# Performance work log

Measured on AMD Instinct MI355X. Metric: run time of the kernel, lower is better.

The kernel has to match this reference:

```python
import jax, jax.numpy as jnp
import numpy as np

N = 100000
E = 1000000
F_IN = 128
HID = 64
HEADS = 4
NC = 4


def setup_inputs() -> dict:
    key = jax.random.key(0)
    ks = jax.random.split(key, 24)
    s = 0.05
    inp = {
        "x": jax.random.normal(ks[0], (N, F_IN), jnp.float32),
        "edge_index": jax.random.randint(ks[1], (2, E), 0, N, jnp.int64 if jax.config.jax_enable_x64 else jnp.int32),
        "edge_weight": jax.random.uniform(ks[2], (E,), jnp.float32),
        "node_mask": jnp.ones((N,), jnp.bool_),
        # GCNConv: lin (no bias applied pre-propagate in math below; bias added after)
        "gcn_W": s * jax.random.normal(ks[3], (F_IN, HID), jnp.float32),
        "gcn_b": jnp.zeros((HID,), jnp.float32),
        "proj_W": s * jax.random.normal(ks[4], (F_IN, HID), jnp.float32),
        "proj_b": jnp.zeros((HID,), jnp.float32),
        "ln1_g": jnp.ones((HID,), jnp.float32), "ln1_b": jnp.zeros((HID,), jnp.float32),
        # GATv2Conv heads=4, concat=False: lin_l, lin_r -> [F, H*C], att [H, C], bias [C]
        "gat_Wl": s * jax.random.normal(ks[5], (HID, HEADS * HID), jnp.float32),
        "gat_Wr": s * jax.random.normal(ks[6], (HID, HEADS * HID), jnp.float32),
        "gat_att": s * jax.random.normal(ks[7], (HEADS, HID), jnp.float32),
        "gat_b": jnp.zeros((HID,), jnp.float32),
        "ln2_g": jnp.ones((HID,), jnp.float32), "ln2_b": jnp.zeros((HID,), jnp.float32),
        # SAGEConv: lin_l (neighbors, with bias), lin_r (root, no bias)
        "sage_Wl": s * jax.random.normal(ks[8], (HID, HID), jnp.float32),
        "sage_bl": jnp.zeros((HID,), jnp.float32),
        "sage_Wr": s * jax.random.normal(ks[9], (HID, HID), jnp.float32),
        "ln3_g": jnp.ones((HID,), jnp.float32), "ln3_b": jnp.zeros((HID,), jnp.float32),
        # edge MLP: Linear(2*HID+1, 32) -> ReLU -> Linear(32, 1)
        "emlp_W1": s * jax.random.normal(ks[10], (2 * HID + 1, 32), jnp.float32),
        "emlp_b1": jnp.zeros((32,), jnp.float32),
        "emlp_W2": s * jax.random.normal(ks[11], (32, 1), jnp.float32),
        "emlp_b2": jnp.zeros((1,), jnp.float32),
        # heads on JK-cat dim 3*HID
        "mort_W": s * jax.random.normal(ks[12], (3 * HID, 1), jnp.float32),
        "mort_b": jnp.zeros((1,), jnp.float32),
        "hours_W": s * jax.random.normal(ks[13], (3 * HID, 1), jnp.float32),
        "hours_b": jnp.zeros((1,), jnp.float32),
        "disc_W": s * jax.random.normal(ks[14], (3 * HID, NC), jnp.float32),
        "disc_b": jnp.zeros((NC,), jnp.float32),
    }
    return inp


def _ln(h, g, b, eps=1e-5):
    mu = jnp.mean(h, axis=-1, keepdims=True)
    var = jnp.mean(jnp.square(h - mu), axis=-1, keepdims=True)
    return (h - mu) * jax.lax.rsqrt(var + eps) * g + b


def reference(x, edge_index, edge_weight, node_mask,
              gcn_W, gcn_b, proj_W, proj_b, ln1_g, ln1_b,
              gat_Wl, gat_Wr, gat_att, gat_b, ln2_g, ln2_b,
              sage_Wl, sage_bl, sage_Wr, ln3_g, ln3_b,
              emlp_W1, emlp_b1, emlp_W2, emlp_b2,
              mort_W, mort_b, hours_W, hours_b, disc_W, disc_b):
    n = x.shape[0]
    src, dst = edge_index[0], edge_index[1]
    loop = jnp.arange(n, dtype=src.dtype)
    s2 = jnp.concatenate([src, loop])  # edges + self loops (GCN, GATv2)
    d2 = jnp.concatenate([dst, loop])

    # ---- GCNConv (normalized, self loops with weight 1) ----
    w2 = jnp.concatenate([edge_weight, jnp.ones((n,), x.dtype)])
    deg = jax.ops.segment_sum(w2, d2, num_segments=n)
    dinv = jnp.where(deg > 0, jax.lax.rsqrt(deg), 0.0)
    norm = dinv[s2] * w2 * dinv[d2]
    xw = x @ gcn_W  # [N, HID]
    gcn_out = jax.ops.segment_sum(norm[:, None] * xw[s2], d2, num_segments=n) + gcn_b
    h1 = jax.nn.relu(_ln(gcn_out, ln1_g, ln1_b))
    h_init = h1 + (x @ proj_W + proj_b)

    # ---- edge-gated edge MLP (recomputed weights; unused by later convs, kept for fidelity) ----
    feat = jnp.concatenate([h_init[src], h_init[dst], edge_weight[:, None]], axis=1)
    _new_ew = jax.nn.sigmoid((jax.nn.relu(feat @ emlp_W1 + emlp_b1) @ emlp_W2 + emlp_b2)[:, 0])

    # ---- GATv2Conv (heads=4, concat=False -> mean over heads, self loops) ----
    H, C = gat_att.shape
    xl = (h_init @ gat_Wl).reshape(n, H, C)
    xr = (h_init @ gat_Wr).reshape(n, H, C)
    e = jax.nn.leaky_relu(xl[s2] + xr[d2], 0.2)        # [E+N, H, C]
    score = jnp.einsum('ehc,hc->eh', e, gat_att)        # [E+N, H]
    smax = jax.ops.segment_max(score, d2, num_segments=n)
    ex = jnp.exp(score - smax[d2])
    den = jax.ops.segment_sum(ex, d2, num_segments=n)
    alpha = ex / den[d2]
    gat_out = jax.ops.segment_sum(alpha[:, :, None] * xl[s2], d2, num_segments=n)
    gat_out = jnp.mean(gat_out, axis=1) + gat_b
    h2 = jax.nn.relu(_ln(gat_out, ln2_g, ln2_b)) + h_init

    # ---- SAGEConv (mean aggregation, root weight, no self loops) ----
    nsum = jax.ops.segment_sum(h2[src], dst, num_segments=n)
    cnt = jax.ops.segment_sum(jnp.ones(src.shape, h2.dtype), dst, num_segments=n)
    nmean = nsum / jnp.maximum(cnt, 1.0)[:, None]
    sage_out = nmean @ sage_Wl + sage_bl + h2 @ sage_Wr
    h3 = jax.nn.relu(_ln(sage_out, ln3_g, ln3_b)) + h2

    # ---- JumpingKnowledge cat + masked readout + heads ----
    x_jk = jnp.concatenate([h_init, h2, h3], axis=1)  # [N, 3*HID]
    readout = jnp.where(node_mask[:, None], x_jk, 0.0)
    mort = (readout @ mort_W + mort_b)[:, 0]
    hours = (readout @ hours_W + hours_b)[:, 0]
    disc = readout @ disc_W + disc_b
    return mort, hours, disc
```

## Files before the change

### kernel.cpp

```cpp
#include <hip/hip_runtime.h>
#include <hip/hip_fp16.h>
#include <math.h>

#define N_NODES 100000
#define N_EDGES 1000000
#define F_IN    128
#define HID     64
#define HEADS   4
#define NCLS    4
#define SCAN_BLK 98
#define GEMM_NT 5

typedef _Float16 half8 __attribute__((ext_vector_type(8)));
typedef _Float16 fp16x2 __attribute__((ext_vector_type(2)));
typedef float f32x4 __attribute__((ext_vector_type(4)));

__device__ __forceinline__ float wsum(float v) {
#pragma unroll
  for (int o = 32; o > 0; o >>= 1) v += __shfl_xor(v, o, 64);
  return v;
}
struct Half4 { __half2 a, b; };
__device__ __forceinline__ __half2 absh2(__half2 v) {
  unsigned u; __builtin_memcpy(&u, &v, 4);
  u &= 0x7FFF7FFFu;
  __half2 r; __builtin_memcpy(&r, &u, 4);
  return r;
}
__device__ __forceinline__ float fdot2f(__half2 a, __half2 b, float c) {
#if defined(__has_builtin) && __has_builtin(__builtin_amdgcn_fdot2)
  fp16x2 av, bv;
  __builtin_memcpy(&av, &a, 4); __builtin_memcpy(&bv, &b, 4);
  return __builtin_amdgcn_fdot2(av, bv, c, false);
#else
  float2 af = __half22float2(a), bf = __half22float2(b);
  return c + af.x * bf.x + af.y * bf.y;
#endif
}
__device__ __forceinline__ float edge_score(Half4 A, __half2 Ra, __half2 Rb,
                                            __half2 at0, __half2 at1,
                                            __half2 c06, __half2 c04) {
  __half2 t0 = __hadd2(A.a, Ra), t1 = __hadd2(A.b, Rb);
  __half2 l0 = __hfma2(t0, c06, __hmul2(absh2(t0), c04));
  __half2 l1 = __hfma2(t1, c06, __hmul2(absh2(t1), c04));
  return fdot2f(l1, at1, fdot2f(l0, at0, 0.f));
}
__device__ __forceinline__ float reduce16(float q) {
  q += __shfl_xor(q, 1); q += __shfl_xor(q, 2);
  q += __shfl_xor(q, 4); q += __shfl_xor(q, 8);
  return q;
}
__device__ __forceinline__ int wave_node() {
  return __builtin_amdgcn_readfirstlane(blockIdx.x * 4 + (threadIdx.x >> 6));
}

__global__ void k_hist(const int* __restrict__ dst, int* __restrict__ cnt) {
  int e = blockIdx.x * 256 + threadIdx.x;
  if (e < N_EDGES) atomicAdd(&cnt[dst[e]], 1);
}
__global__ __launch_bounds__(256) void k_scan1(const int* __restrict__ cnt,
                                               int* __restrict__ partial,
                                               int* __restrict__ bsum) {
  __shared__ int lds[256];
  int t = threadIdx.x;
  int base = blockIdx.x * 1024 + t * 4;
  int v0 = (base + 0 < N_NODES) ? cnt[base + 0] : 0;
  int v1 = (base + 1 < N_NODES) ? cnt[base + 1] : 0;
  int v2 = (base + 2 < N_NODES) ? cnt[base + 2] : 0;
  int v3 = (base + 3 < N_NODES) ? cnt[base + 3] : 0;
  int s = v0 + v1 + v2 + v3;
  lds[t] = s;
  __syncthreads();
  for (int o = 1; o < 256; o <<= 1) {
    int x = (t >= o) ? lds[t - o] : 0;
    __syncthreads();
    lds[t] += x;
    __syncthreads();
  }
  int excl = lds[t] - s;
  if (base + 0 < N_NODES) partial[base + 0] = excl;
  if (base + 1 < N_NODES) partial[base + 1] = excl + v0;
  if (base + 2 < N_NODES) partial[base + 2] = excl + v0 + v1;
  if (base + 3 < N_NODES) partial[base + 3] = excl + v0 + v1 + v2;
  if (t == 255) bsum[blockIdx.x] = lds[255];
}
__global__ void k_scan2(int* __restrict__ bsum) {
  __shared__ int lds[128];
  int t = threadIdx.x;
  int v = (t < SCAN_BLK) ? bsum[t] : 0;
  lds[t] = v;
  __syncthreads();
  for (int o = 1; o < 128; o <<= 1) {
    int x = (t >= o) ? lds[t - o] : 0;
    __syncthreads();
    lds[t] += x;
    __syncthreads();
  }
  if (t < SCAN_BLK) bsum[t] = lds[t] - v;
}
__global__ void k_scan3(const int* __restrict__ partial, const int* __restrict__ bsum,
                        int* __restrict__ row_ptr, int* __restrict__ cursor) {
  int i = blockIdx.x * 256 + threadIdx.x;
  if (i < N_NODES) {
    int v = partial[i] + bsum[i >> 10];
    row_ptr[i] = v;
    cursor[i] = v;
  }
  if (i == 0) row_ptr[N_NODES] = N_EDGES;
}
__global__ void k_fill(const int* __restrict__ src, const int* __restrict__ dst,
                       const float* __restrict__ ew, int* __restrict__ cursor,
                       int* __restrict__ csr_src, float* __restrict__ csr_w) {
  int e = blockIdx.x * 256 + threadIdx.x;
  if (e >= N_EDGES) return;
  int d = dst[e];
  int p = atomicAdd(&cursor[d], 1);
  csr_src[p] = src[e];
  csr_w[p] = ew[e];
}

__global__ __launch_bounds__(512) void k_in_gemm_mfma(
    const float* __restrict__ x, const float* __restrict__ gcn_W,
    const float* __restrict__ proj_W, const float* __restrict__ proj_b,
    __half* __restrict__ xw16, float* __restrict__ xp) {
  __shared__ __half at[16 * 136];
  int t = threadIdx.x;
  int w = t >> 6, lane = t & 63;
  int m = lane & 15, q = lane >> 4;
  int ncol = w * 16 + m;
  const float* W = (ncol < 64) ? gcn_W : proj_W;
  int nc = (ncol < 64) ? ncol : ncol - 64;
  half8 bf[4];
#pragma unroll
  for (int ch = 0; ch < 4; ++ch) {
    int kb = ch * 32 + q * 8;
#pragma unroll
    for (int j = 0; j < 8; ++j)
      bf[ch][j] = (_Float16)W[(kb + j) * 64 + nc];
  }
  float pb = (ncol >= 64) ? proj_b[nc] : 0.f;
  int nb0 = blockIdx.x * (16 * GEMM_NT);
  for (int nt = 0; nt < GEMM_NT; ++nt) {
    int nb = nb0 + nt * 16;
    {
      int row = t >> 5, col = (t & 31) * 4;
      float4 v = *reinterpret_cast<const float4*>(x + (size_t)(nb + row) * F_IN + col);
      __half2* d = reinterpret_cast<__half2*>(&at[row * 136 + col]);
      d[0] = __floats2half2_rn(v.x, v.y);
      d[1] = __floats2half2_rn(v.z, v.w);
    }
    __syncthreads();
    f32x4 acc = {0.f, 0.f, 0.f, 0.f};
#pragma unroll
    for (int ch = 0; ch < 4; ++ch) {
      half8 af = *reinterpret_cast<const half8*>(&at[m * 136 + ch * 32 + q * 8]);
      acc = __builtin_amdgcn_mfma_f32_16x16x32_f16(af, bf[ch], acc, 0, 0, 0);
    }
    if (ncol < 64) {
#pragma unroll
      for (int r = 0; r < 4; ++r)
        xw16[(size_t)(nb + q * 4 + r) * HID + nc] = __float2half(acc[r]);
    } else {
#pragma unroll
      for (int r = 0; r < 4; ++r)
        xp[(size_t)(nb + q * 4 + r) * HID + nc] = acc[r] + pb;
    }
    __syncthreads();
  }
}

__global__ void k_deg(const int* __restrict__ row_ptr, const float* __restrict__ csr_w,
                      float* __restrict__ dinv) {
  int n = blockIdx.x * 256 + threadIdx.x;
  if (n >= N_NODES) return;
  float deg = 1.0f;
  int end = row_ptr[n + 1];
  for (int i = row_ptr[n]; i < end; ++i) deg += csr_w[i];
  dinv[n] = rsqrtf(deg);
}

__global__ __launch_bounds__(256) void k_gcn_fused(
    const int* __restrict__ row_ptr, const int* __restrict__ csr_src,
    const float* __restrict__ csr_w, const float* __restrict__ dinv,
    const __half* __restrict__ xw16, const float* __restrict__ xp,
    const float* __restrict__ gcn_b, const float* __restrict__ g,
    const float* __restrict__ bb, __half* __restrict__ h_init16) {
  int n = wave_node();
  int lane = threadIdx.x & 63;
  float di = dinv[n];
  float acc = di * di * __half2float(xw16[(size_t)n * HID + lane]);
  int beg = row_ptr[n], end = row_ptr[n + 1];
  int i = beg;
  for (; i + 4 <= end; i += 4) {
    int s0 = __builtin_amdgcn_readfirstlane(csr_src[i]);
    int s1 = __builtin_amdgcn_readfirstlane(csr_src[i + 1]);
    int s2 = __builtin_amdgcn_readfirstlane(csr_src[i + 2]);
    int s3 = __builtin_amdgcn_readfirstlane(csr_src[i + 3]);
    float nrm0 = dinv[s0] * csr_w[i] * di;
    float nrm1 = dinv[s1] * csr_w[i + 1] * di;
    float nrm2 = dinv[s2] * csr_w[i + 2] * di;
    float nrm3 = dinv[s3] * csr_w[i + 3] * di;
    float v0 = __half2float(xw16[(size_t)s0 * HID + lane]);
    float v1 = __half2float(xw16[(size_t)s1 * HID + lane]);
    float v2 = __half2float(xw16[(size_t)s2 * HID + lane]);
    float v3 = __half2float(xw16[(size_t)s3 * HID + lane]);
    acc += nrm0 * v0 + nrm1 * v1 + nrm2 * v2 + nrm3 * v3;
  }
  for (; i < end; ++i) {
    int s = __builtin_amdgcn_readfirstlane(csr_src[i]);
    float nrm = dinv[s] * csr_w[i] * di;
    acc += nrm * __half2float(xw16[(size_t)s * HID + lane]);
  }
  float v = acc + gcn_b[lane];
  float mu = wsum(v) * (1.f / HID);
  float dv = v - mu;
  float var = wsum(dv * dv) * (1.f / HID);
  float h = dv * rsqrtf(var + 1e-5f) * g[lane] + bb[lane];
  h = h > 0.f ? h : 0.f;
  h_init16[(size_t)n * HID + lane] = __float2half(h + xp[(size_t)n * HID + lane]);
}

__global__ __launch_bounds__(512) void k_gat_gemm_mfma(
    const __half* __restrict__ h16, const float* __restrict__ Wl,
    const float* __restrict__ Wr, __half* __restrict__ xl, __half* __restrict__ xr) {
  __shared__ __half at[16 * 72];
  int t = threadIdx.x;
  int w = t >> 6, lane = t & 63;
  int m = lane & 15, q = lane >> 4;
  half8 bf[4][2];
#pragma unroll
  for (int tt = 0; tt < 4; ++tt) {
    int c = w * 16 + tt * 128 + m;
    const float* W = (c < 256) ? Wl : Wr;
    int nc = (c < 256) ? c : c - 256;
#pragma unroll
    for (int ch = 0; ch < 2; ++ch) {
      int kb = ch * 32 + q * 8;
#pragma unroll
      for (int j = 0; j < 8; ++j)
        bf[tt][ch][j] = (_Float16)W[(kb + j) * 256 + nc];
    }
  }
  int nb0 = blockIdx.x * (16 * GEMM_NT);
  for (int nt = 0; nt < GEMM_NT; ++nt) {
    int nb = nb0 + nt * 16;
    {
      int row = t >> 5, col = (t & 31) * 2;
      *reinterpret_cast<__half2*>(&at[row * 72 + col]) =
          *reinterpret_cast<const __half2*>(h16 + (size_t)(nb + row) * HID + col);
    }
    __syncthreads();
    half8 a0 = *reinterpret_cast<const half8*>(&at[m * 72 + q * 8]);
    half8 a1 = *reinterpret_cast<const half8*>(&at[m * 72 + 32 + q * 8]);
#pragma unroll
    for (int tt = 0; tt < 4; ++tt) {
      f32x4 acc = {0.f, 0.f, 0.f, 0.f};
      acc = __builtin_amdgcn_mfma_f32_16x16x32_f16(a0, bf[tt][0], acc, 0, 0, 0);
      acc = __builtin_amdgcn_mfma_f32_16x16x32_f16(a1, bf[tt][1], acc, 0, 0, 0);
      int c = w * 16 + tt * 128 + m;
      __half* out = (c < 256) ? (xl + c) : (xr + (c - 256));
#pragma unroll
      for (int r = 0; r < 4; ++r)
        out[(size_t)(nb + q * 4 + r) * 256] = __float2half(acc[r]);
    }
    __syncthreads();
  }
}

__global__ __launch_bounds__(256) void k_gat_fused(
    const int* __restrict__ row_ptr, const int* __restrict__ csr_src,
    const __half* __restrict__ xl, const __half* __restrict__ xr,
    const float* __restrict__ att, const float* __restrict__ gat_b,
    const float* __restrict__ g, const float* __restrict__ bb,
    const __half* __restrict__ h_init16, __half* __restrict__ h2_16) {
  int n = wave_node();
  int lane = threadIdx.x & 63;
  const __half2 c06 = __float2half2_rn(0.6f);
  const __half2 c04 = __float2half2_rn(0.4f);
  float4 atv = *reinterpret_cast<const float4*>(att + lane * 4);
  __half2 at0 = __floats2half2_rn(atv.x, atv.y);
  __half2 at1 = __floats2half2_rn(atv.z, atv.w);
  Half4 R = *reinterpret_cast<const Half4*>(xr + (size_t)n * 256 + lane * 4);
  Half4 S = *reinterpret_cast<const Half4*>(xl + (size_t)n * 256 + lane * 4);

  float q = reduce16(edge_score(S, R.a, R.b, at0, at1, c06, c04));
  float w = __expf(q);
  float den = w;
  float2 f0 = __half22float2(S.a), f1 = __half22float2(S.b);
  float4 acc = make_float4(w * f0.x, w * f0.y, w * f1.x, w * f1.y);

  int beg = row_ptr[n], end = row_ptr[n + 1];
  int i = beg;
  for (; i + 4 <= end; i += 4) {
    int s0 = __builtin_amdgcn_readfirstlane(csr_src[i]);
    int s1 = __builtin_amdgcn_readfirstlane(csr_src[i + 1]);
    int s2 = __builtin_amdgcn_readfirstlane(csr_src[i + 2]);
    int s3 = __builtin_amdgcn_readfirstlane(csr_src[i + 3]);
    Half4 A0 = *reinterpret_cast<const Half4*>(xl + (size_t)s0 * 256 + lane * 4);
    Half4 A1 = *reinterpret_cast<const Half4*>(xl + (size_t)s1 * 256 + lane * 4);
    Half4 A2 = *reinterpret_cast<const Half4*>(xl + (size_t)s2 * 256 + lane * 4);
    Half4 A3 = *reinterpret_cast<const Half4*>(xl + (size_t)s3 * 256 + lane * 4);
    float q0 = edge_score(A0, R.a, R.b, at0, at1, c06, c04);
    float q1 = edge_score(A1, R.a, R.b, at0, at1, c06, c04);
    float q2 = edge_score(A2, R.a, R.b, at0, at1, c06, c04);
    float q3 = edge_score(A3, R.a, R.b, at0, at1, c06, c04);
    q0 += __shfl_xor(q0, 1); q1 += __shfl_xor(q1, 1);
    q2 += __shfl_xor(q2, 1); q3 += __shfl_xor(q3, 1);
    q0 += __shfl_xor(q0, 2); q1 += __shfl_xor(q1, 2);
    q2 += __shfl_xor(q2, 2); q3 += __shfl_xor(q3, 2);
    q0 += __shfl_xor(q0, 4); q1 += __shfl_xor(q1, 4);
    q2 += __shfl_xor(q2, 4); q3 += __shfl_xor(q3, 4);
    q0 += __shfl_xor(q0, 8); q1 += __shfl_xor(q1, 8);
    q2 += __shfl_xor(q2, 8); q3 += __shfl_xor(q3, 8);
    float w0 = __expf(q0), w1 = __expf(q1);
    float w2 = __expf(q2), w3 = __expf(q3);
    den += (w0 + w1) + (w2 + w3);
    float2 a00 = __half22float2(A0.a), a01 = __half22float2(A0.b);
    float2 a10 = __half22float2(A1.a), a11 = __half22float2(A1.b);
    float2 a20 = __half22float2(A2.a), a21 = __half22float2(A2.b);
    float2 a30 = __half22float2(A3.a), a31 = __half22float2(A3.b);
    acc.x += (w0 * a00.x + w1 * a10.x) + (w2 * a20.x + w3 * a30.x);
    acc.y += (w0 * a00.y + w1 * a10.y) + (w2 * a20.y + w3 * a30.y);
    acc.z += (w0 * a01.x + w1 * a11.x) + (w2 * a21.x + w3 * a31.x);
    acc.w += (w0 * a01.y + w1 * a11.y) + (w2 * a21.y + w3 * a31.y);
  }
  for (; i < end; ++i) {
    int s0 = __builtin_amdgcn_readfirstlane(csr_src[i]);
    Half4 A0 = *reinterpret_cast<const Half4*>(xl + (size_t)s0 * 256 + lane * 4);
    q = reduce16(edge_score(A0, R.a, R.b, at0, at1, c06, c04));
    w = __expf(q);
    den += w;
    float2 a00 = __half22float2(A0.a), a01 = __half22float2(A0.b);
    acc.x += w * a00.x; acc.y += w * a00.y;
    acc.z += w * a01.x; acc.w += w * a01.y;
  }
  float inv = 1.f / den;
  acc.x *= inv; acc.y *= inv; acc.z *= inv; acc.w *= inv;
  acc.x += __shfl_xor(acc.x, 16); acc.y += __shfl_xor(acc.y, 16);
  acc.z += __shfl_xor(acc.z, 16); acc.w += __shfl_xor(acc.w, 16);
  acc.x += __shfl_xor(acc.x, 32); acc.y += __shfl_xor(acc.y, 32);
  acc.z += __shfl_xor(acc.z, 32); acc.w += __shfl_xor(acc.w, 32);
  int srcl = lane >> 2;
  float t0 = __shfl(acc.x, srcl), t1 = __shfl(acc.y, srcl);
  float t2 = __shfl(acc.z, srcl), t3 = __shfl(acc.w, srcl);
  int r = lane & 3;
  float mean = (r == 0) ? t0 : (r == 1) ? t1 : (r == 2) ? t2 : t3;
  float val = mean * 0.25f + gat_b[lane];
  float mu = wsum(val) * (1.f / HID);
  float dv = val - mu;
  float var = wsum(dv * dv) * (1.f / HID);
  float h = dv * rsqrtf(var + 1e-5f) * g[lane] + bb[lane];
  h = h > 0.f ? h : 0.f;
  float outv = h + __half2float(h_init16[(size_t)n * HID + lane]);
  h2_16[(size_t)n * HID + lane] = __float2half(outv);
}

__global__ __launch_bounds__(256) void k_sage_gather(
    const int* __restrict__ row_ptr, const int* __restrict__ csr_src,
    const __half* __restrict__ h2_16, float* __restrict__ nmean) {
  int n = wave_node();
  int lane = threadIdx.x & 63;
  int beg = row_ptr[n], end = row_ptr[n + 1];
  float sum = 0.f;
  int i = beg;
  for (; i + 4 <= end; i += 4) {
    int s0 = __builtin_amdgcn_readfirstlane(csr_src[i]);
    int s1 = __builtin_amdgcn_readfirstlane(csr_src[i + 1]);
    int s2 = __builtin_amdgcn_readfirstlane(csr_src[i + 2]);
    int s3 = __builtin_amdgcn_readfirstlane(csr_src[i + 3]);
    float v0 = __half2float(h2_16[(size_t)s0 * HID + lane]);
    float v1 = __half2float(h2_16[(size_t)s1 * HID + lane]);
    float v2 = __half2float(h2_16[(size_t)s2 * HID + lane]);
    float v3 = __half2float(h2_16[(size_t)s3 * HID + lane]);
    sum += v0 + v1 + v2 + v3;
  }
  for (; i < end; ++i) {
    int s = __builtin_amdgcn_readfirstlane(csr_src[i]);
    sum += __half2float(h2_16[(size_t)s * HID + lane]);
  }
  nmean[(size_t)n * HID + lane] = sum / fmaxf((float)(end - beg), 1.f);
}

__global__ __launch_bounds__(64) void k_sage_gemm_ln(
    const float* __restrict__ nmean, const __half* __restrict__ h2_16,
    const float* __restrict__ Wl, const float* __restrict__ Wr,
    const float* __restrict__ sage_bl, const float* __restrict__ g,
    const float* __restrict__ bb, float* __restrict__ h3) {
  __shared__ float nt[8][HID];
  __shared__ float ht[8][HID];
  int t = threadIdx.x;
  int n0 = blockIdx.x * 8;
  {
    const float4* ng = reinterpret_cast<const float4*>(nmean + (size_t)n0 * HID);
    float4* ns = reinterpret_cast<float4*>(&nt[0][0]);
    ns[t] = ng[t];
    ns[t + 64] = ng[t + 64];
    const __half* hp = h2_16 + (size_t)n0 * HID + t * 8;
    Half4 p0 = *reinterpret_cast<const Half4*>(hp);
    Half4 p1 = *reinterpret_cast<const Half4*>(hp + 4);
    float* dsth = &ht[0][0] + t * 8;
    float2 f;
    f = __half22float2(p0.a); dsth[0] = f.x; dsth[1] = f.y;
    f = __half22float2(p0.b); dsth[2] = f.x; dsth[3] = f.y;
    f = __half22float2(p1.a); dsth[4] = f.x; dsth[5] = f.y;
    f = __half22float2(p1.b); dsth[6] = f.x; dsth[7] = f.y;
  }
  __syncthreads();
  int f = t;
  float acc[8] = {0.f,0.f,0.f,0.f,0.f,0.f,0.f,0.f};
  for (int k = 0; k < HID; k += 4) {
    float wl0 = Wl[(k + 0) * HID + f], wr0 = Wr[(k + 0) * HID + f];
    float wl1 = Wl[(k + 1) * HID + f], wr1 = Wr[(k + 1) * HID + f];
    float wl2 = Wl[(k + 2) * HID + f], wr2 = Wr[(k + 2) * HID + f];
    float wl3 = Wl[(k + 3) * HID + f], wr3 = Wr[(k + 3) * HID + f];
#pragma unroll
    for (int j = 0; j < 8; ++j) {
      float4 nv = *reinterpret_cast<const float4*>(&nt[j][k]);
      float4 hv = *reinterpret_cast<const float4*>(&ht[j][k]);
      acc[j] += nv.x * wl0 + nv.y * wl1 + nv.z * wl2 + nv.w * wl3
              + hv.x * wr0 + hv.y * wr1 + hv.z * wr2 + hv.w * wr3;
    }
  }
  float blv = sage_bl[f], gv = g[f], bbv = bb[f];
#pragma unroll
  for (int j = 0; j < 8; ++j) {
    float v = acc[j] + blv;
    float mu = wsum(v) * (1.f / HID);
    float dv = v - mu;
    float var = wsum(dv * dv) * (1.f / HID);
    float h = dv * rsqrtf(var + 1e-5f) * gv + bbv;
    h = h > 0.f ? h : 0.f;
    h3[(size_t)(n0 + j) * HID + f] = h + ht[j][f];
  }
}

__global__ __launch_bounds__(256) void k_heads(
    const __half* __restrict__ h_init16, const __half* __restrict__ h2_16,
    const float* __restrict__ h3, const int* __restrict__ mask,
    const float* __restrict__ mort_W, const float* __restrict__ mort_b,
    const float* __restrict__ hours_W, const float* __restrict__ hours_b,
    const float* __restrict__ disc_W, const float* __restrict__ disc_b,
    float* __restrict__ out) {
  int n = wave_node();
  int lane = threadIdx.x & 63;
  float m = (mask[n] != 0) ? 1.f : 0.f;
  size_t base = (size_t)n * HID;
  float v0 = __half2float(h_init16[base + lane]) * m;
  float v1 = __half2float(h2_16[base + lane]) * m;
  float v2 = h3[base + lane] * m;
  float pm = v0 * mort_W[lane] + v1 * mort_W[64 + lane] + v2 * mort_W[128 + lane];
  float ph = v0 * hours_W[lane] + v1 * hours_W[64 + lane] + v2 * hours_W[128 + lane];
  float d0 = v0 * disc_W[lane * 4 + 0] + v1 * disc_W[(64 + lane) * 4 + 0] + v2 * disc_W[(128 + lane) * 4 + 0];
  float d1 = v0 * disc_W[lane * 4 + 1] + v1 * disc_W[(64 + lane) * 4 + 1] + v2 * disc_W[(128 + lane) * 4 + 1];
  float d2 = v0 * disc_W[lane * 4 + 2] + v1 * disc_W[(64 + lane) * 4 + 2] + v2 * disc_W[(128 + lane) * 4 + 2];
  float d3 = v0 * disc_W[lane * 4 + 3] + v1 * disc_W[(64 + lane) * 4 + 3] + v2 * disc_W[(128 + lane) * 4 + 3];
  pm = wsum(pm); ph = wsum(ph);
  d0 = wsum(d0); d1 = wsum(d1); d2 = wsum(d2); d3 = wsum(d3);
  if (lane == 0) {
    out[n] = pm + mort_b[0];
    out[N_NODES + n] = ph + hours_b[0];
    float* dd = out + 2 * N_NODES + (size_t)n * 4;
    dd[0] = d0 + disc_b[0];
    dd[1] = d1 + disc_b[1];
    dd[2] = d2 + disc_b[2];
    dd[3] = d3 + disc_b[3];
  }
}

extern "C" void kernel_launch(void* const* d_in, const int* in_sizes, int n_in,
                              void* d_out, int out_size, void* d_ws, size_t ws_size,
                              hipStream_t stream) {
  const float* x       = (const float*)d_in[0];
  const int*   ei      = (const int*)d_in[1];
  const float* ew      = (const float*)d_in[2];
  const int*   mask    = (const int*)d_in[3];
  const float* gcn_W   = (const float*)d_in[4];
  const float* gcn_b   = (const float*)d_in[5];
  const float* proj_W  = (const float*)d_in[6];
  const float* proj_b  = (const float*)d_in[7];
  const float* ln1_g   = (const float*)d_in[8];
  const float* ln1_b   = (const float*)d_in[9];
  const float* gat_Wl  = (const float*)d_in[10];
  const float* gat_Wr  = (const float*)d_in[11];
  const float* gat_att = (const float*)d_in[12];
  const float* gat_b   = (const float*)d_in[13];
  const float* ln2_g   = (const float*)d_in[14];
  const float* ln2_b   = (const float*)d_in[15];
  const float* sage_Wl = (const float*)d_in[16];
  const float* sage_bl = (const float*)d_in[17];
  const float* sage_Wr = (const float*)d_in[18];
  const float* ln3_g   = (const float*)d_in[19];
  const float* ln3_b   = (const float*)d_in[20];
  const float* mort_W  = (const float*)d_in[25];
  const float* mort_b  = (const float*)d_in[26];
  const float* hours_W = (const float*)d_in[27];
  const float* hours_b = (const float*)d_in[28];
  const float* disc_W  = (const float*)d_in[29];
  const float* disc_b  = (const float*)d_in[30];

  const int* src = ei;
  const int* dst = ei + N_EDGES;
  float* out = (float*)d_out;

  float* ws = (float*)d_ws;
  const size_t F = (size_t)N_NODES * HID;
  float* h3     = ws + 2 * F;
  float* xp     = h3;
  __half* xl    = (__half*)(ws + 3 * F);
  __half* xw16  = xl;
  float* nmean  = ws + 3 * F;
  __half* xr    = (__half*)(ws + 3 * F + (size_t)N_NODES * 128);
  __half* h2_16 = (__half*)(ws + 3 * F + (size_t)N_NODES * 256);
  __half* h_init16 = (__half*)(ws + 3 * F + (size_t)N_NODES * 288);
  float* tail   = ws + 3 * F + (size_t)N_NODES * 320;
  int*   csr_src = (int*)tail;           tail += N_EDGES;
  float* csr_w   = tail;                 tail += N_EDGES;
  int*   row_ptr = (int*)tail;           tail += N_NODES + 64;
  int*   cursor  = (int*)tail;           tail += N_NODES;
  int*   cnt     = (int*)tail;           tail += N_NODES;
  int*   partial = (int*)tail;           tail += N_NODES;
  int*   bsum    = (int*)tail;           tail += 128;
  float* dinv    = tail;

  const int GE = (N_EDGES + 255) / 256;
  const int GN = (N_NODES + 255) / 256;
  const int GB = N_NODES / (16 * GEMM_NT);

  hipMemsetAsync(cnt, 0, N_NODES * sizeof(int), stream);
  k_hist<<<GE, 256, 0, stream>>>(dst, cnt);
  k_scan1<<<SCAN_BLK, 256, 0, stream>>>(cnt, partial, bsum);
  k_scan2<<<1, 128, 0, stream>>>(bsum);
  k_scan3<<<GN, 256, 0, stream>>>(partial, bsum, row_ptr, cursor);
  k_fill<<<GE, 256, 0, stream>>>(src, dst, ew, cursor, csr_src, csr_w);

  k_in_gemm_mfma<<<GB, 512, 0, stream>>>(x, gcn_W, proj_W, proj_b, xw16, xp);
  k_deg<<<GN, 256, 0, stream>>>(row_ptr, csr_w, dinv);
  k_gcn_fused<<<N_NODES / 4, 256, 0, stream>>>(row_ptr, csr_src, csr_w, dinv, xw16,
                                               xp, gcn_b, ln1_g, ln1_b, h_init16);

  k_gat_gemm_mfma<<<GB, 512, 0, stream>>>(h_init16, gat_Wl, gat_Wr, xl, xr);
  k_gat_fused<<<N_NODES / 4, 256, 0, stream>>>(row_ptr, csr_src, xl, xr, gat_att,
                                               gat_b, ln2_g, ln2_b, h_init16, h2_16);

  k_sage_gather<<<N_NODES / 4, 256, 0, stream>>>(row_ptr, csr_src, h2_16, nmean);
  k_sage_gemm_ln<<<N_NODES / 8, 64, 0, stream>>>(nmean, h2_16, sage_Wl, sage_Wr,
                                                 sage_bl, ln3_g, ln3_b, h3);

  k_heads<<<N_NODES / 4, 256, 0, stream>>>(h_init16, h2_16, h3, mask, mort_W, mort_b,
                                           hours_W, hours_b, disc_W, disc_b, out);
}
```

Baseline: 571.7 us.

## Fuse readout heads into SAGE GEMM, fold scan2 into scan3, store fp16 intermediates

Merges the block-sum scan into the final scan kernel, so each block rescans the 98 block sums in LDS and one launch is dropped. The projection output and the SAGE neighbour mean are now stored as fp16 instead of fp32, which halves their memory traffic. The heads kernel is fused into the SAGE GEMM+LayerNorm kernel, so h3 is never written to or read back from global memory. The cost is lower precision on two intermediates and redundant scan work in every scan3 block.

Measured after the change: 566.4 us. No clear change (-0.9%).

```diff
diff --git a/kernel.cpp b/kernel.cpp
--- a/kernel.cpp
+++ b/kernel.cpp
@@ -84,25 +84,29 @@
   if (base + 3 < N_NODES) partial[base + 3] = excl + v0 + v1 + v2;
   if (t == 255) bsum[blockIdx.x] = lds[255];
 }
-__global__ void k_scan2(int* __restrict__ bsum) {
-  __shared__ int lds[128];
+__global__ __launch_bounds__(256) void k_scan3(const int* __restrict__ partial,
+                                               const int* __restrict__ bsum,
+                                               int* __restrict__ row_ptr,
+                                               int* __restrict__ cursor) {
+  __shared__ int ex[128];
   int t = threadIdx.x;
-  int v = (t < SCAN_BLK) ? bsum[t] : 0;
-  lds[t] = v;
+  int orig = 0;
+  if (t < 128) {
+    orig = (t < SCAN_BLK) ? bsum[t] : 0;
+    ex[t] = orig;
+  }
   __syncthreads();
   for (int o = 1; o < 128; o <<= 1) {
-    int x = (t >= o) ? lds[t - o] : 0;
-    __syncthreads();
-    lds[t] += x;
-    __syncthreads();
-  }
-  if (t < SCAN_BLK) bsum[t] = lds[t] - v;
-}
-__global__ void k_scan3(const int* __restrict__ partial, const int* __restrict__ bsum,
-                        int* __restrict__ row_ptr, int* __restrict__ cursor) {
-  int i = blockIdx.x * 256 + threadIdx.x;
+    int x = (t < 128 && t >= o) ? ex[t - o] : 0;
+    __syncthreads();
+    if (t < 128) ex[t] += x;
+    __syncthreads();
+  }
+  if (t < 128) ex[t] -= orig;
+  __syncthreads();
+  int i = blockIdx.x * 256 + t;
   if (i < N_NODES) {
-    int v = partial[i] + bsum[i >> 10];
+    int v = partial[i] + ex[i >> 10];
     row_ptr[i] = v;
     cursor[i] = v;
   }
@@ -122,7 +126,7 @@
 __global__ __launch_bounds__(512) void k_in_gemm_mfma(
     const float* __restrict__ x, const float* __restrict__ gcn_W,
     const float* __restrict__ proj_W, const float* __restrict__ proj_b,
-    __half* __restrict__ xw16, float* __restrict__ xp) {
+    __half* __restrict__ xw16, __half* __restrict__ xp16) {
   __shared__ __half at[16 * 136];
   int t = threadIdx.x;
   int w = t >> 6, lane = t & 63;
@@ -163,7 +167,7 @@
     } else {
 #pragma unroll
       for (int r = 0; r < 4; ++r)
-        xp[(size_t)(nb + q * 4 + r) * HID + nc] = acc[r] + pb;
+        xp16[(size_t)(nb + q * 4 + r) * HID + nc] = __float2half(acc[r] + pb);
     }
     __syncthreads();
   }
@@ -182,7 +186,7 @@
 __global__ __launch_bounds__(256) void k_gcn_fused(
     const int* __restrict__ row_ptr, const int* __restrict__ csr_src,
     const float* __restrict__ csr_w, const float* __restrict__ dinv,
-    const __half* __restrict__ xw16, const float* __restrict__ xp,
+    const __half* __restrict__ xw16, const __half* __restrict__ xp16,
     const float* __restrict__ gcn_b, const float* __restrict__ g,
     const float* __restrict__ bb, __half* __restrict__ h_init16) {
   int n = wave_node();
@@ -217,7 +221,8 @@
   float var = wsum(dv * dv) * (1.f / HID);
   float h = dv * rsqrtf(var + 1e-5f) * g[lane] + bb[lane];
   h = h > 0.f ? h : 0.f;
-  h_init16[(size_t)n * HID + lane] = __float2half(h + xp[(size_t)n * HID + lane]);
+  h_init16[(size_t)n * HID + lane] =
+      __float2half(h + __half2float(xp16[(size_t)n * HID + lane]));
 }
 
 __global__ __launch_bounds__(512) void k_gat_gemm_mfma(
@@ -357,7 +362,7 @@
 
 __global__ __launch_bounds__(256) void k_sage_gather(
     const int* __restrict__ row_ptr, const int* __restrict__ csr_src,
-    const __half* __restrict__ h2_16, float* __restrict__ nmean) {
+    const __half* __restrict__ h2_16, __half* __restrict__ nmean16) {
   int n = wave_node();
   int lane = threadIdx.x & 63;
   int beg = row_ptr[n], end = row_ptr[n + 1];
@@ -378,32 +383,42 @@
     int s = __builtin_amdgcn_readfirstlane(csr_src[i]);
     sum += __half2float(h2_16[(size_t)s * HID + lane]);
   }
-  nmean[(size_t)n * HID + lane] = sum / fmaxf((float)(end - beg), 1.f);
-}
-
-__global__ __launch_bounds__(64) void k_sage_gemm_ln(
-    const float* __restrict__ nmean, const __half* __restrict__ h2_16,
+  nmean16[(size_t)n * HID + lane] =
+      __float2half(sum / fmaxf((float)(end - beg), 1.f));
+}
+
+__global__ __launch_bounds__(64) void k_sage_gemm_ln_heads(
+    const __half* __restrict__ nmean16, const __half* __restrict__ h2_16,
+    const __half* __restrict__ h_init16,
     const float* __restrict__ Wl, const float* __restrict__ Wr,
     const float* __restrict__ sage_bl, const float* __restrict__ g,
-    const float* __restrict__ bb, float* __restrict__ h3) {
+    const float* __restrict__ bb, const int* __restrict__ mask,
+    const float* __restrict__ mort_W, const float* __restrict__ mort_b,
+    const float* __restrict__ hours_W, const float* __restrict__ hours_b,
+    const float* __restrict__ disc_W, const float* __restrict__ disc_b,
+    float* __restrict__ out) {
   __shared__ float nt[8][HID];
   __shared__ float ht[8][HID];
   int t = threadIdx.x;
   int n0 = blockIdx.x * 8;
   {
-    const float4* ng = reinterpret_cast<const float4*>(nmean + (size_t)n0 * HID);
-    float4* ns = reinterpret_cast<float4*>(&nt[0][0]);
-    ns[t] = ng[t];
-    ns[t + 64] = ng[t + 64];
+    const __half* np = nmean16 + (size_t)n0 * HID + t * 8;
     const __half* hp = h2_16 + (size_t)n0 * HID + t * 8;
+    Half4 n0v = *reinterpret_cast<const Half4*>(np);
+    Half4 n1v = *reinterpret_cast<const Half4*>(np + 4);
     Half4 p0 = *reinterpret_cast<const Half4*>(hp);
     Half4 p1 = *reinterpret_cast<const Half4*>(hp + 4);
-    float* dsth = &ht[0][0] + t * 8;
+    float* dn = &nt[0][0] + t * 8;
+    float* dh = &ht[0][0] + t * 8;
     float2 f;
-    f = __half22float2(p0.a); dsth[0] = f.x; dsth[1] = f.y;
-    f = __half22float2(p0.b); dsth[2] = f.x; dsth[3] = f.y;
-    f = __half22float2(p1.a); dsth[4] = f.x; dsth[5] = f.y;
-    f = __half22float2(p1.b); dsth[6] = f.x; dsth[7] = f.y;
+    f = __half22float2(n0v.a); dn[0] = f.x; dn[1] = f.y;
+    f = __half22float2(n0v.b); dn[2] = f.x; dn[3] = f.y;
+    f = __half22float2(n1v.a); dn[4] = f.x; dn[5] = f.y;
+    f = __half22float2(n1v.b); dn[6] = f.x; dn[7] = f.y;
+    f = __half22float2(p0.a);  dh[0] = f.x; dh[1] = f.y;
+    f = __half22float2(p0.b);  dh[2] = f.x; dh[3] = f.y;
+    f = __half22float2(p1.a);  dh[4] = f.x; dh[5] = f.y;
+    f = __half22float2(p1.b);  dh[6] = f.x; dh[7] = f.y;
   }
   __syncthreads();
   int f = t;
@@ -422,6 +437,14 @@
     }
   }
   float blv = sage_bl[f], gv = g[f], bbv = bb[f];
+  float mw0 = mort_W[f], mw1 = mort_W[64 + f], mw2 = mort_W[128 + f];
+  float hw0 = hours_W[f], hw1 = hours_W[64 + f], hw2 = hours_W[128 + f];
+  float dwv[12];
+#pragma unroll
+  for (int rr = 0; rr < 3; ++rr)
+#pragma unroll
+    for (int c = 0; c < 4; ++c)
+      dwv[rr * 4 + c] = disc_W[(rr * 64 + f) * 4 + c];
 #pragma unroll
   for (int j = 0; j < 8; ++j) {
     float v = acc[j] + blv;
@@ -430,40 +453,28 @@
     float var = wsum(dv * dv) * (1.f / HID);
     float h = dv * rsqrtf(var + 1e-5f) * gv + bbv;
     h = h > 0.f ? h : 0.f;
-    h3[(size_t)(n0 + j) * HID + f] = h + ht[j][f];
-  }
-}
-
-__global__ __launch_bounds__(256) void k_heads(
-    const __half* __restrict__ h_init16, const __half* __restrict__ h2_16,
-    const float* __restrict__ h3, const int* __restrict__ mask,
-    const float* __restrict__ mort_W, const float* __restrict__ mort_b,
-    const float* __restrict__ hours_W, const float* __restrict__ hours_b,
-    const float* __restrict__ disc_W, const float* __restrict__ disc_b,
-    float* __restrict__ out) {
-  int n = wave_node();
-  int lane = threadIdx.x & 63;
-  float m = (mask[n] != 0) ? 1.f : 0.f;
-  size_t base = (size_t)n * HID;
-  float v0 = __half2float(h_init16[base + lane]) * m;
-  float v1 = __half2float(h2_16[base + lane]) * m;
-  float v2 = h3[base + lane] * m;
-  float pm = v0 * mort_W[lane] + v1 * mort_W[64 + lane] + v2 * mort_W[128 + lane];
-  float ph = v0 * hours_W[lane] + v1 * hours_W[64 + lane] + v2 * hours_W[128 + lane];
-  float d0 = v0 * disc_W[lane * 4 + 0] + v1 * disc_W[(64 + lane) * 4 + 0] + v2 * disc_W[(128 + lane) * 4 + 0];
-  float d1 = v0 * disc_W[lane * 4 + 1] + v1 * disc_W[(64 + lane) * 4 + 1] + v2 * disc_W[(128 + lane) * 4 + 1];
-  float d2 = v0 * disc_W[lane * 4 + 2] + v1 * disc_W[(64 + lane) * 4 + 2] + v2 * disc_W[(128 + lane) * 4 + 2];
-  float d3 = v0 * disc_W[lane * 4 + 3] + v1 * disc_W[(64 + lane) * 4 + 3] + v2 * disc_W[(128 + lane) * 4 + 3];
-  pm = wsum(pm); ph = wsum(ph);
-  d0 = wsum(d0); d1 = wsum(d1); d2 = wsum(d2); d3 = wsum(d3);
-  if (lane == 0) {
-    out[n] = pm + mort_b[0];
-    out[N_NODES + n] = ph + hours_b[0];
-    float* dd = out + 2 * N_NODES + (size_t)n * 4;
-    dd[0] = d0 + disc_b[0];
-    dd[1] = d1 + disc_b[1];
-    dd[2] = d2 + disc_b[2];
-    dd[3] = d3 + disc_b[3];
+    int n = n0 + j;
+    float m = (mask[n] != 0) ? 1.f : 0.f;
+    float v2 = (h + ht[j][f]) * m;
+    float v1 = ht[j][f] * m;
+    float v0 = __half2float(h_init16[(size_t)n * HID + f]) * m;
+    float pm = v0 * mw0 + v1 * mw1 + v2 * mw2;
+    float ph = v0 * hw0 + v1 * hw1 + v2 * hw2;
+    float d0 = v0 * dwv[0] + v1 * dwv[4] + v2 * dwv[8];
+    float d1 = v0 * dwv[1] + v1 * dwv[5] + v2 * dwv[9];
+    float d2 = v0 * dwv[2] + v1 * dwv[6] + v2 * dwv[10];
+    float d3 = v0 * dwv[3] + v1 * dwv[7] + v2 * dwv[11];
+    pm = wsum(pm); ph = wsum(ph);
+    d0 = wsum(d0); d1 = wsum(d1); d2 = wsum(d2); d3 = wsum(d3);
+    if (f == 0) {
+      out[n] = pm + mort_b[0];
+      out[N_NODES + n] = ph + hours_b[0];
+      float* dd = out + 2 * N_NODES + (size_t)n * 4;
+      dd[0] = d0 + disc_b[0];
+      dd[1] = d1 + disc_b[1];
+      dd[2] = d2 + disc_b[2];
+      dd[3] = d3 + disc_b[3];
+    }
   }
 }
 
@@ -504,11 +515,10 @@
 
   float* ws = (float*)d_ws;
   const size_t F = (size_t)N_NODES * HID;
-  float* h3     = ws + 2 * F;
-  float* xp     = h3;
+  __half* xp16  = (__half*)(ws + 2 * F);
   __half* xl    = (__half*)(ws + 3 * F);
   __half* xw16  = xl;
-  float* nmean  = ws + 3 * F;
+  __half* nmean16 = (__half*)(ws + 3 * F);
   __half* xr    = (__half*)(ws + 3 * F + (size_t)N_NODES * 128);
   __half* h2_16 = (__half*)(ws + 3 * F + (size_t)N_NODES * 256);
   __half* h_init16 = (__half*)(ws + 3 * F + (size_t)N_NODES * 288);
@@ -529,23 +539,20 @@
   hipMemsetAsync(cnt, 0, N_NODES * sizeof(int), stream);
   k_hist<<<GE, 256, 0, stream>>>(dst, cnt);
   k_scan1<<<SCAN_BLK, 256, 0, stream>>>(cnt, partial, bsum);
-  k_scan2<<<1, 128, 0, stream>>>(bsum);
   k_scan3<<<GN, 256, 0, stream>>>(partial, bsum, row_ptr, cursor);
   k_fill<<<GE, 256, 0, stream>>>(src, dst, ew, cursor, csr_src, csr_w);
 
-  k_in_gemm_mfma<<<GB, 512, 0, stream>>>(x, gcn_W, proj_W, proj_b, xw16, xp);
+  k_in_gemm_mfma<<<GB, 512, 0, stream>>>(x, gcn_W, proj_W, proj_b, xw16, xp16);
   k_deg<<<GN, 256, 0, stream>>>(row_ptr, csr_w, dinv);
   k_gcn_fused<<<N_NODES / 4, 256, 0, stream>>>(row_ptr, csr_src, csr_w, dinv, xw16,
-                                               xp, gcn_b, ln1_g, ln1_b, h_init16);
+                                               xp16, gcn_b, ln1_g, ln1_b, h_init16);
 
   k_gat_gemm_mfma<<<GB, 512, 0, stream>>>(h_init16, gat_Wl, gat_Wr, xl, xr);
   k_gat_fused<<<N_NODES / 4, 256, 0, stream>>>(row_ptr, csr_src, xl, xr, gat_att,
                                                gat_b, ln2_g, ln2_b, h_init16, h2_16);
 
-  k_sage_gather<<<N_NODES / 4, 256, 0, stream>>>(row_ptr, csr_src, h2_16, nmean);
-  k_sage_gemm_ln<<<N_NODES / 8, 64, 0, stream>>>(nmean, h2_16, sage_Wl, sage_Wr,
-                                                 sage_bl, ln3_g, ln3_b, h3);
-
-  k_heads<<<N_NODES / 4, 256, 0, stream>>>(h_init16, h2_16, h3, mask, mort_W, mort_b,
-                                           hours_W, hours_b, disc_W, disc_b, out);
-}
+  k_sage_gather<<<N_NODES / 4, 256, 0, stream>>>(row_ptr, csr_src, h2_16, nmean16);
+  k_sage_gemm_ln_heads<<<N_NODES / 8, 64, 0, stream>>>(
+      nmean16, h2_16, h_init16, sage_Wl, sage_Wr, sage_bl, ln3_g, ln3_b, mask,
+      mort_W, mort_b, hours_W, hours_b, disc_W, disc_b, out);
+}
```
